# Kernel optimization log

Hardware: AMD Instinct MI355X
Metric: run time of the kernel (lower is better)

Reference implementation:

```python
import jax, jax.numpy as jnp
import numpy as np

EPS = 1e-5
NUM_GROUPS = 16


def _deform_conv(x, offset, mask, weight):
    """Modulated deformable conv v2, 3x3, stride 1, pad 1, no bias.
    x: [B,C,H,W], offset: [B,18,H,W] (y,x interleaved per kernel point),
    mask: [B,9,H,W], weight: [O,C,3,3].
    """
    B, C, H, W = x.shape
    O = weight.shape[0]
    K = 9
    off = offset.reshape(B, K, 2, H, W)
    dy, dx = off[:, :, 0], off[:, :, 1]  # [B,K,H,W]
    # base sampling grid: output pixel + kernel tap offset (pad=1 -> taps -1..1)
    ky, kx = jnp.meshgrid(jnp.arange(3), jnp.arange(3), indexing='ij')
    ky = (ky.reshape(K) - 1).astype(x.dtype)
    kx = (kx.reshape(K) - 1).astype(x.dtype)
    iy = jnp.arange(H, dtype=x.dtype)[:, None]
    ix = jnp.arange(W, dtype=x.dtype)[None, :]
    py = iy[None, None] + ky[None, :, None, None] + dy  # [B,K,H,W]
    px = ix[None, None] + kx[None, :, None, None] + dx

    y0 = jnp.floor(py)
    x0 = jnp.floor(px)
    wy = py - y0  # grad flows to offsets via these weights
    wx = px - x0

    xf = x.reshape(B, C, H * W)

    def gather(yc, xc, w):
        # yc,xc,w: [B,K,H,W] float; returns weighted samples [B,C,K,H,W]
        valid = (yc >= 0) & (yc <= H - 1) & (xc >= 0) & (xc <= W - 1)
        yi = jnp.clip(yc, 0, H - 1).astype(jnp.int32)
        xi = jnp.clip(xc, 0, W - 1).astype(jnp.int32)
        idx = (yi * W + xi).reshape(B, K * H * W)
        g = jax.vmap(lambda xb, ib: xb[:, ib])(xf, idx)  # [B,C,K*H*W]
        g = g.reshape(B, C, K, H, W)
        wv = (w * valid.astype(x.dtype))[:, None]  # [B,1,K,H,W]
        return g * wv

    val = gather(y0, x0, (1 - wy) * (1 - wx))
    val = val + gather(y0, x0 + 1, (1 - wy) * wx)
    val = val + gather(y0 + 1, x0, wy * (1 - wx))
    val = val + gather(y0 + 1, x0 + 1, wy * wx)

    val = val * mask[:, None]  # modulation: [B,C,K,H,W] * [B,1,K,H,W]
    w = weight.reshape(O, C, K)
    return jnp.einsum('bckhw,ock->bohw', val, w)


def _group_norm(y, gamma, beta):
    B, O, H, W = y.shape
    g = y.reshape(B, NUM_GROUPS, O // NUM_GROUPS, H, W)
    mean = g.mean(axis=(2, 3, 4), keepdims=True)
    var = ((g - mean) ** 2).mean(axis=(2, 3, 4), keepdims=True)
    g = (g - mean) * jax.lax.rsqrt(var + EPS)
    y = g.reshape(B, O, H, W)
    return y * gamma[None, :, None, None] + beta[None, :, None, None]


def setup_inputs() -> dict:
    key = jax.random.key(0)
    k1, k2, k3, k4 = jax.random.split(key, 4)
    B, C, O, H, W = 8, 256, 256, 64, 64
    x = jax.random.normal(k1, (B, C, H, W), jnp.float32)
    offset = jax.random.normal(k2, (B, 18, H, W), jnp.float32)
    mask = jax.random.uniform(k3, (B, 9, H, W), jnp.float32)
    weight = jax.random.normal(k4, (O, C, 3, 3), jnp.float32) * 0.02
    gamma = jnp.ones((O,), jnp.float32)
    beta = jnp.zeros((O,), jnp.float32)
    return {"x": x, "offset": offset, "mask": mask, "weight": weight,
            "gamma": gamma, "beta": beta}


def reference(x, offset, mask, weight, gamma, beta):
    y = _deform_conv(x, offset, mask, weight)
    return _group_norm(y, gamma, beta)
```

## Files before the change

### kernel.cpp

```cpp
#include <hip/hip_runtime.h>
#include <hip/hip_fp16.h>
#include <math.h>

#define BB 8
#define CC 256
#define OO 256
#define HH 64
#define WW 64
#define KK 9
#define HWSZ 4096
#define CKSZ 2304
#define NG 16
#define OPG 16
#define EPSV 1e-5f

typedef _Float16 f16;
typedef f16 f16x8 __attribute__((ext_vector_type(8)));
typedef float f32x4 __attribute__((ext_vector_type(4)));

#define XH_ELEMS ((size_t)BB*HWSZ*CC)
#define WF_ELEMS ((size_t)OO*CKSZ)
#define CV_ELEMS ((size_t)BB*OO*HWSZ)
#define NSTRIP 32

__global__ __launch_bounds__(256) void x_transpose_k(
    const float* __restrict__ x, __half* __restrict__ xh)
{
  int blk = blockIdx.x;
  int b = blk >> 8; int rem = blk & 255;
  int c0 = (rem >> 6) * 64; int hw0 = (rem & 63) * 64;
  __shared__ float st[64][65];
  int t = threadIdx.x;
  #pragma unroll
  for (int i = 0; i < 16; ++i) {
    int idx = t + i*256; int c = idx >> 6, w = idx & 63;
    st[c][w] = x[((size_t)(b*CC + c0 + c))*HWSZ + hw0 + w];
  }
  __syncthreads();
  #pragma unroll
  for (int i = 0; i < 8; ++i) {
    int idx = t + i*256; int r = idx >> 5, cp = idx & 31;
    __half2 v = __floats2half2_rn(st[cp*2][r], st[cp*2+1][r]);
    *(__half2*)&xh[((size_t)(b*HWSZ) + hw0 + r)*CC + c0 + cp*2] = v;
  }
}

__global__ __launch_bounds__(256) void w_frag_k(
    const float* __restrict__ w, __half* __restrict__ wf)
{
  int i = blockIdx.x*256 + threadIdx.x;
  int e = i & 7, lane = (i >> 3) & 63, mi = (i >> 9) & 3;
  int ks = (i >> 11) & 1, wm = (i >> 12) & 3, cc = i >> 14;
  int k = cc >> 2, c0i = cc & 3;
  int o = wm*64 + mi*16 + (lane & 15);
  int c = c0i*64 + ks*32 + (lane >> 4)*8 + e;
  wf[i] = __float2half(w[(o*CC + c)*KK + k]);
}

template<int F16OUT>
__global__ __launch_bounds__(1024, 4) void dcn_mfma_k(
    const float* __restrict__ off, const float* __restrict__ msk,
    const __half* __restrict__ xh, const __half* __restrict__ wf,
    float* __restrict__ out32, __half* __restrict__ conv16,
    float* __restrict__ psum)
{
  __shared__ __half sVl[4][128*64];

  const int t = threadIdx.x;
  const int b = blockIdx.x & 7;
  const int strip = blockIdx.x >> 3;
  const int h0 = strip * 2;

  const int lane = t & 63, wid = t >> 6;
  const int lr = lane & 15, lh = lane >> 4;
  const int gp = t >> 3, goct = t & 7;

  auto load_A = [&](int cc, f16x8 a[2]) {
    #pragma unroll
    for (int ks = 0; ks < 2; ++ks) {
      const __half* ap = wf + (size_t)(cc*4 + (wid >> 2))*4096
                            + (size_t)(ks*4 + (wid & 3))*512 + lane*8;
      a[ks] = *(const f16x8*)ap;
    }
  };

  f16x8 aregA[2], aregB[2];
  load_A(0, aregA);
  load_A(1, aregB);

  f32x4 acc[8];
  #pragma unroll
  for (int ni = 0; ni < 8; ++ni) acc[ni] = (f32x4){0.f,0.f,0.f,0.f};

  const char* xbase = (const char*)xh + (size_t)b * (HWSZ*CC*2);

  uint toff[4]; __half2 twv[4];
  auto compute_taps = [&](int k) {
    int h = h0 + (gp >> 6), w = gp & 63;
    float dy = off[(((b*18) + 2*k    )*HH + h)*WW + w];
    float dx = off[(((b*18) + 2*k + 1)*HH + h)*WW + w];
    float m  = msk[(((b*KK) + k)*HH + h)*WW + w];
    float py = (float)(h + (k/3) - 1) + dy;
    float px = (float)(w + (k%3) - 1) + dx;
    float y0f = floorf(py), x0f = floorf(px);
    float wy = py - y0f, wx = px - x0f;
    int y0 = (int)y0f, x0 = (int)x0f;
    #pragma unroll
    for (int tap = 0; tap < 4; ++tap) {
      int yy = y0 + (tap >> 1), xx = x0 + (tap & 1);
      bool v = (yy >= 0) & (yy < HH) & (xx >= 0) & (xx < WW);
      float bw = ((tap >> 1) ? wy : 1.f - wy) * ((tap & 1) ? wx : 1.f - wx);
      float wgt = v ? bw * m : 0.f;
      int cy = min(max(yy, 0), HH-1), cx = min(max(xx, 0), WW-1);
      toff[tap] = (uint)((cy*WW + cx) * (CC*2));
      twv[tap]  = __float2half2_rn(wgt);
    }
  };
  int tk = 0;
  compute_taps(0);

  auto combine_write = [&](uint4 r0, uint4 r1, uint4 r2, uint4 r3,
                           __half* dst) {
    const __half2* t0 = (const __half2*)&r0; const __half2* t1 = (const __half2*)&r1;
    const __half2* t2 = (const __half2*)&r2; const __half2* t3 = (const __half2*)&r3;
    __half2 o_[4];
    #pragma unroll
    for (int r = 0; r < 4; ++r)
      o_[r] = __hfma2(twv[0], t0[r], __hfma2(twv[1], t1[r],
              __hfma2(twv[2], t2[r], __hmul2(twv[3], t3[r]))));
    *(uint4*)&dst[gp*64 + ((goct ^ (gp & 7)) << 3)] = *(uint4*)o_;
  };

  auto gather_chunk = [&](int cc, __half* dst) {
    int kn = cc >> 2, c0n = (cc & 3) << 6;
    if (kn != tk) { compute_taps(kn); tk = kn; }
    const char* cb = xbase + (size_t)(c0n*2) + goct*16;
    uint4 r0 = *(const uint4*)(cb + toff[0]);
    uint4 r1 = *(const uint4*)(cb + toff[1]);
    uint4 r2 = *(const uint4*)(cb + toff[2]);
    uint4 r3 = *(const uint4*)(cb + toff[3]);
    combine_write(r0, r1, r2, r3, dst);
  };

  gather_chunk(0, sVl[0]);
  gather_chunk(1, sVl[1]);

  auto do_half = [&](int ccm, int ccf, f16x8 aCur[2]) {
    bool pf = (ccf < 36);
    int kn = ccf >> 2, c0n = (ccf & 3) << 6;
    uint4 g0, g1, g2, g3;
    if (pf) {
      if (kn != tk) { compute_taps(kn); tk = kn; }
      const char* cb = xbase + (size_t)(c0n*2) + goct*16;
      g0 = *(const uint4*)(cb + toff[0]);
      g1 = *(const uint4*)(cb + toff[1]);
      g2 = *(const uint4*)(cb + toff[2]);
      g3 = *(const uint4*)(cb + toff[3]);
    }

    const __half* vb = sVl[ccm & 3];
    #pragma unroll
    for (int ks = 0; ks < 2; ++ks) {
      f16x8 brg[8];
      #pragma unroll
      for (int ni = 0; ni < 8; ++ni) {
        int r = ni*16 + lr;
        brg[ni] = *(const f16x8*)&vb[r*64 + (((ks*4 + lh) ^ (r & 7)) << 3)];
      }
      #pragma unroll
      for (int ni = 0; ni < 8; ++ni)
        acc[ni] = __builtin_amdgcn_mfma_f32_16x16x32_f16(
            aCur[ks], brg[ni], acc[ni], 0, 0, 0);
    }

    if (pf) {
      combine_write(g0, g1, g2, g3, sVl[ccf & 3]);
      load_A(ccf, aCur);
    }
  };

  #pragma unroll 1
  for (int ccp = 0; ccp < 36; ccp += 2) {
    __syncthreads();
    do_half(ccp,     ccp + 2, aregA);
    do_half(ccp + 1, ccp + 3, aregB);
  }

  #pragma unroll
  for (int ni = 0; ni < 8; ++ni) {
    int pp = ni*16 + lr;
    #pragma unroll
    for (int j = 0; j < 4; ++j) {
      int o = wid*16 + lh*4 + j;
      size_t idx = ((size_t)(b*OO + o))*HWSZ + strip*128 + pp;
      if (F16OUT) conv16[idx] = __float2half(acc[ni][j]);
      else        out32[idx] = acc[ni][j];
    }
  }

  if (F16OUT) {
    float s1 = 0.f, s2 = 0.f;
    #pragma unroll
    for (int ni = 0; ni < 8; ++ni)
      #pragma unroll
      for (int j = 0; j < 4; ++j) {
        float v = acc[ni][j];
        s1 += v; s2 += v*v;
      }
    #pragma unroll
    for (int d = 32; d > 0; d >>= 1) {
      s1 += __shfl_xor(s1, d);
      s2 += __shfl_xor(s2, d);
    }
    if (lane == 0) {
      psum[(size_t)blockIdx.x*32 + wid*2]     = s1;
      psum[(size_t)blockIdx.x*32 + wid*2 + 1] = s2;
    }
  }
}

__global__ __launch_bounds__(256) void gn_norm2_k(
    const __half* __restrict__ conv16, const float* __restrict__ psum,
    const float* __restrict__ gamma, const float* __restrict__ beta,
    float* __restrict__ out)
{
  int bid = blockIdx.x;
  int bo = bid >> 1;
  int b = bo >> 8, o = bo & 255;
  int g = o >> 4;
  float s1 = 0.f, s2 = 0.f;
  for (int st = 0; st < NSTRIP; ++st) {
    s1 += psum[(size_t)(st*8 + b)*32 + g*2];
    s2 += psum[(size_t)(st*8 + b)*32 + g*2 + 1];
  }
  const float invN = 1.f / (float)(OPG*HWSZ);
  float mean = s1 * invN;
  float var  = s2 * invN - mean*mean;
  float inv = rsqrtf(var + EPSV);
  float sc = gamma[o]*inv;
  float sh = beta[o] - mean*sc;

  size_t e0 = ((size_t)(b*OO + o))*HWSZ + (size_t)(bid & 1)*2048
            + (size_t)threadIdx.x*8;
  uint4 u = *(const uint4*)(conv16 + e0);
  const __half2* hh = (const __half2*)&u;
  float r[8];
  #pragma unroll
  for (int j = 0; j < 4; ++j) {
    float2 f = __half22float2(hh[j]);
    r[2*j] = f.x; r[2*j+1] = f.y;
  }
  *(float4*)&out[e0]     = make_float4(r[0]*sc+sh, r[1]*sc+sh, r[2]*sc+sh, r[3]*sc+sh);
  *(float4*)&out[e0 + 4] = make_float4(r[4]*sc+sh, r[5]*sc+sh, r[6]*sc+sh, r[7]*sc+sh);
}

__global__ __launch_bounds__(1024) void gn_stats_k(
    const float* __restrict__ out, float* __restrict__ stats)
{
  int bg = blockIdx.x;
  const float4* p = (const float4*)(out + (size_t)bg*OPG*HWSZ);
  const int n4 = OPG*HWSZ/4;
  float s1 = 0.f, s2 = 0.f;
  for (int i = threadIdx.x; i < n4; i += 1024) {
    float4 v = p[i];
    s1 += v.x + v.y + v.z + v.w;
    s2 += v.x*v.x + v.y*v.y + v.z*v.z + v.w*v.w;
  }
  #pragma unroll
  for (int o2 = 32; o2 > 0; o2 >>= 1) {
    s1 += __shfl_down(s1, o2);
    s2 += __shfl_down(s2, o2);
  }
  __shared__ float r1[16], r2[16];
  int wd = threadIdx.x >> 6, lane = threadIdx.x & 63;
  if (lane == 0) { r1[wd] = s1; r2[wd] = s2; }
  __syncthreads();
  if (threadIdx.x == 0) {
    float t1 = 0.f, t2 = 0.f;
    #pragma unroll
    for (int i = 0; i < 16; i++) { t1 += r1[i]; t2 += r2[i]; }
    const float invN = 1.f / (float)(OPG*HWSZ);
    float mean = t1 * invN;
    float var  = t2 * invN - mean*mean;
    stats[bg*2]   = mean;
    stats[bg*2+1] = var;
  }
}

__global__ __launch_bounds__(256) void gn_norm_k(
    float* __restrict__ out, const float* __restrict__ stats,
    const float* __restrict__ gamma, const float* __restrict__ beta)
{
  size_t i = (size_t)blockIdx.x*256 + threadIdx.x;
  const size_t n4 = (size_t)BB*OO*HWSZ/4;
  if (i >= n4) return;
  size_t base = i*4;
  int bo = (int)(base / HWSZ);
  int b = bo / OO, o = bo - b*OO;
  int g = o >> 4;
  float mean = stats[(b*NG+g)*2], var = stats[(b*NG+g)*2+1];
  float inv = rsqrtf(var + EPSV);
  float sc = gamma[o]*inv;
  float sh = beta[o] - mean*sc;
  float4 v = *(float4*)&out[base];
  v.x = v.x*sc + sh; v.y = v.y*sc + sh;
  v.z = v.z*sc + sh; v.w = v.w*sc + sh;
  *(float4*)&out[base] = v;
}

extern "C" void kernel_launch(void* const* d_in, const int* in_sizes, int n_in,
                              void* d_out, int out_size, void* d_ws, size_t ws_size,
                              hipStream_t stream) {
  const float* x      = (const float*)d_in[0];
  const float* offset = (const float*)d_in[1];
  const float* mask   = (const float*)d_in[2];
  const float* weight = (const float*)d_in[3];
  const float* gamma  = (const float*)d_in[4];
  const float* beta   = (const float*)d_in[5];
  float* out = (float*)d_out;

  __half* xh   = (__half*)d_ws;
  __half* wf   = xh + XH_ELEMS;
  __half* cv   = wf + WF_ELEMS;
  float* psum  = (float*)(cv + CV_ELEMS);

  const size_t need = (XH_ELEMS + WF_ELEMS + CV_ELEMS)*2
                    + (size_t)BB*NSTRIP*32*4 + 1024;

  x_transpose_k<<<BB*4*64, 256, 0, stream>>>(x, xh);
  w_frag_k<<<(int)(WF_ELEMS/256), 256, 0, stream>>>(weight, wf);

  if (ws_size >= need) {
    dcn_mfma_k<1><<<BB*NSTRIP, 1024, 0, stream>>>(offset, mask, xh, wf,
                                                  (float*)nullptr, cv, psum);
    gn_norm2_k<<<4096, 256, 0, stream>>>(cv, psum, gamma, beta, out);
  } else {
    float* stats = (float*)(wf + WF_ELEMS);
    dcn_mfma_k<0><<<BB*NSTRIP, 1024, 0, stream>>>(offset, mask, xh, wf,
                                                  out, (__half*)nullptr,
                                                  (float*)nullptr);
    gn_stats_k<<<BB*NG, 1024, 0, stream>>>(out, stats);
    gn_norm_k<<<(int)((size_t)BB*OO*HWSZ/4 + 255)/256, 256, 0, stream>>>(
        out, stats, gamma, beta);
  }
}
```

Before: 83.10 us.

## Retile MFMA warp layout to 2x4 output tiles per wave for operand reuse

Each wave now computes a 32-output by 64-pixel tile (2 M-tiles x 4 N-tiles) instead of 16 outputs by 128 pixels. This halves the LDS B-fragment reads per wave and reuses each B fragment across two A fragments, at the cost of twice as many weight fragment loads per wave. Group-norm partial sums are now combined across the two pixel-half waves through shared memory, which adds an extra block barrier at the end.

```diff
diff --git a/kernel.cpp b/kernel.cpp
--- a/kernel.cpp
+++ b/kernel.cpp
@@ -65,6 +65,7 @@
     float* __restrict__ psum)
 {
   __shared__ __half sVl[4][128*64];
+  __shared__ float  sRedG[8][2][2][2];
 
   const int t = threadIdx.x;
   const int b = blockIdx.x & 7;
@@ -72,25 +73,31 @@
   const int h0 = strip * 2;
 
   const int lane = t & 63, wid = t >> 6;
+  const int wo = wid & 7, wp = wid >> 3;
   const int lr = lane & 15, lh = lane >> 4;
   const int gp = t >> 3, goct = t & 7;
 
-  auto load_A = [&](int cc, f16x8 a[2]) {
-    #pragma unroll
-    for (int ks = 0; ks < 2; ++ks) {
-      const __half* ap = wf + (size_t)(cc*4 + (wid >> 2))*4096
-                            + (size_t)(ks*4 + (wid & 3))*512 + lane*8;
-      a[ks] = *(const f16x8*)ap;
-    }
-  };
-
-  f16x8 aregA[2], aregB[2];
+  auto load_A = [&](int cc, f16x8 a[2][2]) {
+    #pragma unroll
+    for (int ks = 0; ks < 2; ++ks)
+      #pragma unroll
+      for (int mi = 0; mi < 2; ++mi) {
+        int omi = wo*2 + mi;
+        const __half* ap = wf + (size_t)(cc*4 + (omi >> 2))*4096
+                              + (size_t)(ks*4 + (omi & 3))*512 + lane*8;
+        a[ks][mi] = *(const f16x8*)ap;
+      }
+  };
+
+  f16x8 aregA[2][2], aregB[2][2];
   load_A(0, aregA);
   load_A(1, aregB);
 
-  f32x4 acc[8];
-  #pragma unroll
-  for (int ni = 0; ni < 8; ++ni) acc[ni] = (f32x4){0.f,0.f,0.f,0.f};
+  f32x4 acc[2][4];
+  #pragma unroll
+  for (int mi = 0; mi < 2; ++mi)
+    #pragma unroll
+    for (int ni = 0; ni < 4; ++ni) acc[mi][ni] = (f32x4){0.f,0.f,0.f,0.f};
 
   const char* xbase = (const char*)xh + (size_t)b * (HWSZ*CC*2);
 
@@ -145,7 +152,7 @@
   gather_chunk(0, sVl[0]);
   gather_chunk(1, sVl[1]);
 
-  auto do_half = [&](int ccm, int ccf, f16x8 aCur[2]) {
+  auto do_half = [&](int ccm, int ccf, f16x8 aCur[2][2]) {
     bool pf = (ccf < 36);
     int kn = ccf >> 2, c0n = (ccf & 3) << 6;
     uint4 g0, g1, g2, g3;
@@ -161,16 +168,18 @@
     const __half* vb = sVl[ccm & 3];
     #pragma unroll
     for (int ks = 0; ks < 2; ++ks) {
-      f16x8 brg[8];
-      #pragma unroll
-      for (int ni = 0; ni < 8; ++ni) {
-        int r = ni*16 + lr;
+      f16x8 brg[4];
+      #pragma unroll
+      for (int ni = 0; ni < 4; ++ni) {
+        int r = wp*64 + ni*16 + lr;
         brg[ni] = *(const f16x8*)&vb[r*64 + (((ks*4 + lh) ^ (r & 7)) << 3)];
       }
       #pragma unroll
-      for (int ni = 0; ni < 8; ++ni)
-        acc[ni] = __builtin_amdgcn_mfma_f32_16x16x32_f16(
-            aCur[ks], brg[ni], acc[ni], 0, 0, 0);
+      for (int mi = 0; mi < 2; ++mi)
+        #pragma unroll
+        for (int ni = 0; ni < 4; ++ni)
+          acc[mi][ni] = __builtin_amdgcn_mfma_f32_16x16x32_f16(
+              aCur[ks][mi], brg[ni], acc[mi][ni], 0, 0, 0);
     }
 
     if (pf) {
@@ -187,34 +196,47 @@
   }
 
   #pragma unroll
-  for (int ni = 0; ni < 8; ++ni) {
-    int pp = ni*16 + lr;
-    #pragma unroll
-    for (int j = 0; j < 4; ++j) {
-      int o = wid*16 + lh*4 + j;
-      size_t idx = ((size_t)(b*OO + o))*HWSZ + strip*128 + pp;
-      if (F16OUT) conv16[idx] = __float2half(acc[ni][j]);
-      else        out32[idx] = acc[ni][j];
+  for (int mi = 0; mi < 2; ++mi) {
+    #pragma unroll
+    for (int ni = 0; ni < 4; ++ni) {
+      int o  = wo*32 + mi*16 + lh*4;
+      int pp = wp*64 + ni*16 + lr;
+      #pragma unroll
+      for (int j = 0; j < 4; ++j) {
+        size_t idx = ((size_t)(b*OO + o + j))*HWSZ + strip*128 + pp;
+        if (F16OUT) conv16[idx] = __float2half(acc[mi][ni][j]);
+        else        out32[idx] = acc[mi][ni][j];
+      }
     }
   }
 
   if (F16OUT) {
-    float s1 = 0.f, s2 = 0.f;
-    #pragma unroll
-    for (int ni = 0; ni < 8; ++ni)
-      #pragma unroll
-      for (int j = 0; j < 4; ++j) {
-        float v = acc[ni][j];
-        s1 += v; s2 += v*v;
-      }
-    #pragma unroll
-    for (int d = 32; d > 0; d >>= 1) {
-      s1 += __shfl_xor(s1, d);
-      s2 += __shfl_xor(s2, d);
-    }
-    if (lane == 0) {
-      psum[(size_t)blockIdx.x*32 + wid*2]     = s1;
-      psum[(size_t)blockIdx.x*32 + wid*2 + 1] = s2;
+    #pragma unroll
+    for (int mi = 0; mi < 2; ++mi) {
+      float s1 = 0.f, s2 = 0.f;
+      #pragma unroll
+      for (int ni = 0; ni < 4; ++ni)
+        #pragma unroll
+        for (int j = 0; j < 4; ++j) {
+          float v = acc[mi][ni][j];
+          s1 += v; s2 += v*v;
+        }
+      #pragma unroll
+      for (int d = 32; d > 0; d >>= 1) {
+        s1 += __shfl_xor(s1, d);
+        s2 += __shfl_xor(s2, d);
+      }
+      if (lane == 0) {
+        sRedG[wo][mi][wp][0] = s1;
+        sRedG[wo][mi][wp][1] = s2;
+      }
+    }
+    __syncthreads();
+    if (t < 16) {
+      float s1 = sRedG[t >> 1][t & 1][0][0] + sRedG[t >> 1][t & 1][1][0];
+      float s2 = sRedG[t >> 1][t & 1][0][1] + sRedG[t >> 1][t & 1][1][1];
+      psum[(size_t)blockIdx.x*32 + t*2]     = s1;
+      psum[(size_t)blockIdx.x*32 + t*2 + 1] = s2;
     }
   }
 }
```

Result: slower. 91.10 us (+9.6%).
